# Performance work log

Hardware: AMD Instinct MI355X
Metric: run time of the kernel (lower is better)

Reference implementation:

```python
import jax, jax.numpy as jnp
import numpy as np

N_NODES = 50000


def _sage_mean(x, src, dst, Wl, bl, Wr, n_nodes):
    # PyG SAGEConv (aggr='mean', root_weight=True): lin_l(mean_j x_j) + lin_r(x_i)
    msgs = x[src]                                             # [E, F] gather
    agg = jax.ops.segment_sum(msgs, dst, num_segments=n_nodes)  # [N, F]
    cnt = jax.ops.segment_sum(jnp.ones((src.shape[0],), x.dtype), dst,
                              num_segments=n_nodes)           # [N]
    mean = agg / jnp.maximum(cnt, 1.0)[:, None]
    return mean @ Wl + bl + x @ Wr


def setup_inputs() -> dict:
    key = jax.random.key(0)
    ks = jax.random.split(key, 12)
    in_ft = 64
    o0, o1, o2 = 64, 128, 128
    d2 = o0 + o0          # conv2 in = 128
    d3 = o0 + o0 + o1     # conv3 in = 256
    E = 800000

    def lin(k, fi, fo):
        s = 1.0 / np.sqrt(fi)
        return jax.random.uniform(k, (fi, fo), jnp.float32, -s, s)

    x = jax.random.normal(ks[0], (N_NODES, in_ft), jnp.float32)
    edge_index = jax.random.randint(ks[1], (2, E), 0, N_NODES, jnp.int64)
    return {
        "x": x,
        "edge_index": edge_index,
        "Wp": lin(ks[2], in_ft, o0), "bp": jnp.zeros((o0,), jnp.float32),
        "Wl1": lin(ks[3], in_ft, o0), "bl1": jnp.zeros((o0,), jnp.float32),
        "Wr1": lin(ks[4], in_ft, o0),
        "Wl2": lin(ks[5], d2, o1), "bl2": jnp.zeros((o1,), jnp.float32),
        "Wr2": lin(ks[6], d2, o1),
        "Wl3": lin(ks[7], d3, o2), "bl3": jnp.zeros((o2,), jnp.float32),
        "Wr3": lin(ks[8], d3, o2),
    }


def reference(x, edge_index, Wp, bp, Wl1, bl1, Wr1, Wl2, bl2, Wr2, Wl3, bl3, Wr3):
    src, dst = edge_index[0], edge_index[1]
    act = jax.nn.relu
    x_p = act(x @ Wp + bp)                                        # [N, o0]
    h1 = act(_sage_mean(x, src, dst, Wl1, bl1, Wr1, N_NODES))      # [N, o0]
    in2 = jnp.concatenate([x_p, h1], axis=1)                      # [N, 2*o0]
    h2 = act(_sage_mean(in2, src, dst, Wl2, bl2, Wr2, N_NODES))    # [N, o1]
    in3 = jnp.concatenate([x_p, h1, h2], axis=1)                  # [N, 2*o0+o1]
    h3 = act(_sage_mean(in3, src, dst, Wl3, bl3, Wr3, N_NODES))    # [N, o2]
    return h3
```

## Files before the change

kernel.cpp:

```cpp
#include <hip/hip_runtime.h>

#define N_NODES 50000
#define ELLW 48
#define BINCAP 131072

typedef unsigned int uint;
typedef unsigned short ushort;
typedef float floatx4 __attribute__((ext_vector_type(4)));
typedef short short8 __attribute__((ext_vector_type(8)));

__device__ inline ushort f2bf(float f) {
    uint u = __float_as_uint(f);
    return (ushort)((u + 0x7fffu + ((u >> 16) & 1u)) >> 16);
}
__device__ inline float bflo(uint u) { return __uint_as_float(u << 16); }
__device__ inline float bfhi(uint u) { return __uint_as_float(u & 0xffff0000u); }

__device__ inline void swz_body(const float* __restrict__ W, ushort* __restrict__ Wz,
                                int O, int t) {
    int lane = t & 63, cb = t >> 6;
    int NBm = O / 16;
    int c = cb / NBm, nb = cb % NBm;
    int quad = lane >> 4, l16 = lane & 15;
#pragma unroll
    for (int j = 0; j < 8; j++) {
        float v = W[(size_t)(c * 32 + quad * 8 + j) * O + nb * 16 + l16];
        Wz[(size_t)t * 8 + j] = f2bf(v);
    }
}

__device__ void gemm1_body(int gb, const float* __restrict__ x,
                           const float* __restrict__ Wp, const float* __restrict__ bp,
                           ushort* __restrict__ feats, ushort* ldsA) {
    constexpr int LDA = 40;
    const int tid = threadIdx.x;
    const int wave = tid >> 6, lane = tid & 63;
    const int quad = lane >> 4, l16 = lane & 15;
    const int node0 = gb * 64;

    floatx4 acc[4];
#pragma unroll
    for (int nb = 0; nb < 4; nb++) acc[nb] = (floatx4){0, 0, 0, 0};

#pragma unroll
    for (int kk = 0; kk < 2; kk++) {
        const int k0 = kk * 32;
        __syncthreads();
        {
            int row = tid >> 2, seg = tid & 3;
            int node = node0 + row;
            float4 v0 = {0, 0, 0, 0}, v1 = {0, 0, 0, 0};
            if (node < N_NODES) {
                v0 = *(const float4*)&x[(size_t)node * 64 + k0 + seg * 8];
                v1 = *(const float4*)&x[(size_t)node * 64 + k0 + seg * 8 + 4];
            }
            ushort4 o0, o1;
            o0.x = f2bf(v0.x); o0.y = f2bf(v0.y); o0.z = f2bf(v0.z); o0.w = f2bf(v0.w);
            o1.x = f2bf(v1.x); o1.y = f2bf(v1.y); o1.z = f2bf(v1.z); o1.w = f2bf(v1.w);
            *(ushort4*)&ldsA[row * LDA + seg * 8] = o0;
            *(ushort4*)&ldsA[row * LDA + seg * 8 + 4] = o1;
        }
        __syncthreads();

        short8 a = *(const short8*)&ldsA[(wave * 16 + l16) * LDA + quad * 8];
#pragma unroll
        for (int nb = 0; nb < 4; nb++) {
            short8 bw;
#pragma unroll
            for (int j = 0; j < 8; j++)
                bw[j] = (short)f2bf(Wp[(size_t)(k0 + quad * 8 + j) * 64 + nb * 16 + l16]);
            acc[nb] = __builtin_amdgcn_mfma_f32_16x16x32_bf16(a, bw, acc[nb], 0, 0, 0);
        }
    }

#pragma unroll
    for (int nb = 0; nb < 4; nb++) {
        int ncol = nb * 16 + l16;
        float bv = bp[ncol];
#pragma unroll
        for (int r = 0; r < 4; r++) {
            int node = node0 + wave * 16 + quad * 4 + r;
            if (node >= N_NODES) continue;
            feats[(size_t)node * 256 + ncol] = f2bf(fmaxf(acc[nb][r] + bv, 0.f));
        }
    }
}

__global__ __launch_bounds__(256) void k1_mega(
    const int* __restrict__ src, const int* __restrict__ dst, int E,
    uint* __restrict__ bins, int* __restrict__ binCnt, int* __restrict__ fillc,
    const float* __restrict__ x, ushort* __restrict__ xb,
    const float* __restrict__ Wp, const float* __restrict__ bp, ushort* __restrict__ feats,
    const float* __restrict__ Wl1, ushort* __restrict__ zl1,
    const float* __restrict__ Wr1, ushort* __restrict__ zr1,
    const float* __restrict__ Wl2, ushort* __restrict__ zl2,
    const float* __restrict__ Wr2, ushort* __restrict__ zr2,
    const float* __restrict__ Wl3, ushort* __restrict__ zl3,
    const float* __restrict__ Wr3, ushort* __restrict__ zr3,
    int NA, int NG, int NC, int NZ)
{
    __shared__ ushort ldsA[64 * 40];
    __shared__ int cnt[8], base[8];
    int b = blockIdx.x, tid = threadIdx.x;

    if (b < NA) {
        int t = b * 256 + tid;
        bool valid = t < E;
        int s = 0, d = 0, bin = 0;
        if (valid) { s = src[t]; d = dst[t]; bin = d / 6250; }
        if (tid < 8) cnt[tid] = 0;
        __syncthreads();
        int rank = 0;
        if (valid) rank = atomicAdd(&cnt[bin], 1);
        __syncthreads();
        if (tid < 8) base[tid] = atomicAdd(&binCnt[tid], cnt[tid]);
        __syncthreads();
        if (valid)
            bins[(size_t)bin * BINCAP + base[bin] + rank] = (uint)s | ((uint)d << 16);
        return;
    }
    b -= NA;
    if (b < NG) { gemm1_body(b, x, Wp, bp, feats, ldsA); return; }
    b -= NG;
    if (b < NC) {
        int t = b * 256 + tid;
        float4 v = ((const float4*)x)[t];
        ushort4 o;
        o.x = f2bf(v.x); o.y = f2bf(v.y); o.z = f2bf(v.z); o.w = f2bf(v.w);
        ((ushort4*)xb)[t] = o;
        return;
    }
    b -= NC;
    if (b < NZ) {
        int t = b * 256 + tid;
        if (t < 12500) ((uint4*)fillc)[t] = (uint4){0, 0, 0, 0};
        return;
    }
    b -= NZ;
    if      (b < 2)  swz_body(Wl1, zl1, 64,  (b - 0) * 256 + tid);
    else if (b < 4)  swz_body(Wr1, zr1, 64,  (b - 2) * 256 + tid);
    else if (b < 12) swz_body(Wl2, zl2, 128, (b - 4) * 256 + tid);
    else if (b < 20) swz_body(Wr2, zr2, 128, (b - 12) * 256 + tid);
    else if (b < 36) swz_body(Wl3, zl3, 128, (b - 20) * 256 + tid);
    else             swz_body(Wr3, zr3, 128, (b - 36) * 256 + tid);
}

__global__ __launch_bounds__(256) void scatter_k(const uint* __restrict__ bins,
                                                 const int* __restrict__ binCnt,
                                                 int* __restrict__ fillc,
                                                 ushort* __restrict__ ell) {
    int bin = blockIdx.x & 7;
    int sub = blockIdx.x >> 3;
    int n = binCnt[bin];
    const uint* bp = bins + (size_t)bin * BINCAP;
    for (int i = sub * 256 + threadIdx.x; i < n; i += 64 * 256) {
        uint pk = bp[i];
        int s = pk & 0xFFFF, d = pk >> 16;
        int p = atomicAdd(&fillc[d], 1);
        if (p < ELLW) ell[(size_t)d * ELLW + p] = (ushort)s;
    }
}


__global__ __launch_bounds__(256) void gather64_k(const int* __restrict__ fillc,
                                                  const ushort* __restrict__ ell,
                                                  const ushort* __restrict__ in,
                                                  ushort* __restrict__ out) {
    int wid = blockIdx.x * 4 + (threadIdx.x >> 6);
    int lane = threadIdx.x & 63;
    int half = lane >> 5;
    int node = wid * 2 + half;
    if (node >= N_NODES) return;
    int l32 = lane & 31;
    int sub = l32 >> 3, c = l32 & 7;
    int n = fillc[node]; int nc = (n > ELLW) ? ELLW : n;
    const ushort* base = ell + (size_t)node * ELLW;
    float a[8];
#pragma unroll
    for (int j = 0; j < 8; j++) a[j] = 0.f;

    int i = sub;
    for (; i + 12 < nc; i += 16) {
        uint4 u0 = *(const uint4*)&in[(size_t)base[i] * 64 + 8 * c];
        uint4 u1 = *(const uint4*)&in[(size_t)base[i + 4] * 64 + 8 * c];
        uint4 u2 = *(const uint4*)&in[(size_t)base[i + 8] * 64 + 8 * c];
        uint4 u3 = *(const uint4*)&in[(size_t)base[i + 12] * 64 + 8 * c];
        a[0] += (bflo(u0.x) + bflo(u1.x)) + (bflo(u2.x) + bflo(u3.x));
        a[1] += (bfhi(u0.x) + bfhi(u1.x)) + (bfhi(u2.x) + bfhi(u3.x));
        a[2] += (bflo(u0.y) + bflo(u1.y)) + (bflo(u2.y) + bflo(u3.y));
        a[3] += (bfhi(u0.y) + bfhi(u1.y)) + (bfhi(u2.y) + bfhi(u3.y));
        a[4] += (bflo(u0.z) + bflo(u1.z)) + (bflo(u2.z) + bflo(u3.z));
        a[5] += (bfhi(u0.z) + bfhi(u1.z)) + (bfhi(u2.z) + bfhi(u3.z));
        a[6] += (bflo(u0.w) + bflo(u1.w)) + (bflo(u2.w) + bflo(u3.w));
        a[7] += (bfhi(u0.w) + bfhi(u1.w)) + (bfhi(u2.w) + bfhi(u3.w));
    }
    for (; i < nc; i += 4) {
        uint4 u0 = *(const uint4*)&in[(size_t)base[i] * 64 + 8 * c];
        a[0] += bflo(u0.x);  a[1] += bfhi(u0.x);
        a[2] += bflo(u0.y);  a[3] += bfhi(u0.y);
        a[4] += bflo(u0.z);  a[5] += bfhi(u0.z);
        a[6] += bflo(u0.w);  a[7] += bfhi(u0.w);
    }
#pragma unroll
    for (int j = 0; j < 8; j++) {
        a[j] += __shfl_xor(a[j], 8);
        a[j] += __shfl_xor(a[j], 16);
    }
    if (sub == 0) {
        float iv = 1.0f / fmaxf((float)n, 1.0f);
        uint4 r;
        r.x = (uint)f2bf(a[0] * iv) | ((uint)f2bf(a[1] * iv) << 16);
        r.y = (uint)f2bf(a[2] * iv) | ((uint)f2bf(a[3] * iv) << 16);
        r.z = (uint)f2bf(a[4] * iv) | ((uint)f2bf(a[5] * iv) << 16);
        r.w = (uint)f2bf(a[6] * iv) | ((uint)f2bf(a[7] * iv) << 16);
        *(uint4*)&out[(size_t)node * 64 + 8 * c] = r;
    }
}

__global__ __launch_bounds__(256) void gather128_k(const int* __restrict__ fillc,
                                                   const ushort* __restrict__ ell,
                                                   const ushort* __restrict__ in,
                                                   ushort* __restrict__ out) {
    int node = blockIdx.x * 4 + (threadIdx.x >> 6);
    if (node >= N_NODES) return;
    int lane = threadIdx.x & 63;
    int sub = lane >> 4, c = lane & 15;
    int n = fillc[node]; int nc = (n > ELLW) ? ELLW : n;
    const ushort* base = ell + (size_t)node * ELLW;
    float a[8];
#pragma unroll
    for (int j = 0; j < 8; j++) a[j] = 0.f;

    int i = sub;
    for (; i + 12 < nc; i += 16) {
        uint4 u0 = *(const uint4*)&in[(size_t)base[i] * 256 + 8 * c];
        uint4 u1 = *(const uint4*)&in[(size_t)base[i + 4] * 256 + 8 * c];
        uint4 u2 = *(const uint4*)&in[(size_t)base[i + 8] * 256 + 8 * c];
        uint4 u3 = *(const uint4*)&in[(size_t)base[i + 12] * 256 + 8 * c];
        a[0] += (bflo(u0.x) + bflo(u1.x)) + (bflo(u2.x) + bflo(u3.x));
        a[1] += (bfhi(u0.x) + bfhi(u1.x)) + (bfhi(u2.x) + bfhi(u3.x));
        a[2] += (bflo(u0.y) + bflo(u1.y)) + (bflo(u2.y) + bflo(u3.y));
        a[3] += (bfhi(u0.y) + bfhi(u1.y)) + (bfhi(u2.y) + bfhi(u3.y));
        a[4] += (bflo(u0.z) + bflo(u1.z)) + (bflo(u2.z) + bflo(u3.z));
        a[5] += (bfhi(u0.z) + bfhi(u1.z)) + (bfhi(u2.z) + bfhi(u3.z));
        a[6] += (bflo(u0.w) + bflo(u1.w)) + (bflo(u2.w) + bflo(u3.w));
        a[7] += (bfhi(u0.w) + bfhi(u1.w)) + (bfhi(u2.w) + bfhi(u3.w));
    }
    for (; i < nc; i += 4) {
        uint4 u0 = *(const uint4*)&in[(size_t)base[i] * 256 + 8 * c];
        a[0] += bflo(u0.x);  a[1] += bfhi(u0.x);
        a[2] += bflo(u0.y);  a[3] += bfhi(u0.y);
        a[4] += bflo(u0.z);  a[5] += bfhi(u0.z);
        a[6] += bflo(u0.w);  a[7] += bfhi(u0.w);
    }
#pragma unroll
    for (int j = 0; j < 8; j++) {
        a[j] += __shfl_xor(a[j], 16);
        a[j] += __shfl_xor(a[j], 32);
    }
    if (sub == 0) {
        float iv = 1.0f / fmaxf((float)n, 1.0f);
        uint4 r;
        r.x = (uint)f2bf(a[0] * iv) | ((uint)f2bf(a[1] * iv) << 16);
        r.y = (uint)f2bf(a[2] * iv) | ((uint)f2bf(a[3] * iv) << 16);
        r.z = (uint)f2bf(a[4] * iv) | ((uint)f2bf(a[5] * iv) << 16);
        r.w = (uint)f2bf(a[6] * iv) | ((uint)f2bf(a[7] * iv) << 16);
        *(uint4*)&out[(size_t)node * 256 + 8 * c] = r;
    }
}


template <int O, bool OUT_BF16>
__global__ __launch_bounds__(256) void mfma_gemm_k(
    const ushort* __restrict__ A1, int s1, int K1, const ushort* __restrict__ Wz1,
    const ushort* __restrict__ A2, int s2, int K2, const ushort* __restrict__ Wz2,
    const float* __restrict__ bias, void* __restrict__ outp, int so, int ocol)
{
    constexpr int NB = O / 16;
    constexpr int LDA = 40;
    __shared__ ushort ldsA[64 * LDA];

    const int tid = threadIdx.x;
    const int wave = tid >> 6, lane = tid & 63;
    const int quad = lane >> 4, l16 = lane & 15;
    const int node0 = blockIdx.x * 64;

    floatx4 acc[NB];
#pragma unroll
    for (int nb = 0; nb < NB; nb++) acc[nb] = (floatx4){0, 0, 0, 0};

#pragma unroll 1
    for (int phase = 0; phase < 2; ++phase) {
        const ushort* A = phase ? A2 : A1;
        const ushort* Wz = phase ? Wz2 : Wz1;
        const int K = phase ? K2 : K1;
        const int sA = phase ? s2 : s1;

#pragma unroll 1
        for (int k0 = 0; k0 < K; k0 += 32) {
            __syncthreads();
            {
                int row = tid >> 2, seg = tid & 3;
                int node = node0 + row;
                uint4 v = {0, 0, 0, 0};
                if (node < N_NODES)
                    v = *(const uint4*)&A[(size_t)node * sA + k0 + seg * 8];
                *(uint4*)&ldsA[row * LDA + seg * 8] = v;
            }
            __syncthreads();

            short8 a = *(const short8*)&ldsA[(wave * 16 + l16) * LDA + quad * 8];
            const short8* bz = (const short8*)Wz + (size_t)(k0 >> 5) * NB * 64;
#pragma unroll
            for (int nb = 0; nb < NB; nb++) {
                short8 b = bz[nb * 64 + lane];
                acc[nb] = __builtin_amdgcn_mfma_f32_16x16x32_bf16(a, b, acc[nb], 0, 0, 0);
            }
        }
    }

#pragma unroll
    for (int nb = 0; nb < NB; nb++) {
        int ncol = nb * 16 + l16;
        float bv = bias[ncol];
#pragma unroll
        for (int r = 0; r < 4; r++) {
            int node = node0 + wave * 16 + quad * 4 + r;
            if (node >= N_NODES) continue;
            float v = fmaxf(acc[nb][r] + bv, 0.f);
            if (OUT_BF16)
                ((ushort*)outp)[(size_t)node * so + ocol + ncol] = f2bf(v);
            else
                ((float*)outp)[(size_t)node * so + ocol + ncol] = v;
        }
    }
}


extern "C" void kernel_launch(void* const* d_in, const int* in_sizes, int n_in,
                              void* d_out, int out_size, void* d_ws, size_t ws_size,
                              hipStream_t stream) {
    const float* x   = (const float*)d_in[0];
    const int*   ei  = (const int*)d_in[1];
    const float* Wp  = (const float*)d_in[2];
    const float* bp  = (const float*)d_in[3];
    const float* Wl1 = (const float*)d_in[4];
    const float* bl1 = (const float*)d_in[5];
    const float* Wr1 = (const float*)d_in[6];
    const float* Wl2 = (const float*)d_in[7];
    const float* bl2 = (const float*)d_in[8];
    const float* Wr2 = (const float*)d_in[9];
    const float* Wl3 = (const float*)d_in[10];
    const float* bl3 = (const float*)d_in[11];
    const float* Wr3 = (const float*)d_in[12];

    const int E = in_sizes[1] / 2;
    const int N = N_NODES;
    const int* src = ei;
    const int* dst = ei + E;

    char* p = (char*)d_ws;
    ushort* xb    = (ushort*)p;  p += (size_t)N * 64 * 2;
    ushort* feats = (ushort*)p;  p += (size_t)N * 256 * 2;
    ushort* aggx  = (ushort*)p;  p += (size_t)N * 64 * 2;
    ushort* aggf  = (ushort*)p;  p += (size_t)N * 256 * 2;
    int* fillc    = (int*)p;     p += (size_t)N * 4;
    ushort* ell   = (ushort*)p;  p += (size_t)N * ELLW * 2;
    uint* bins    = (uint*)p;    p += (size_t)8 * BINCAP * 4;
    int* binCnt   = (int*)p;     p += 16 * 4;
    ushort* zl1   = (ushort*)p;  p += 64 * 64 * 2;
    ushort* zr1   = (ushort*)p;  p += 64 * 64 * 2;
    ushort* zl2   = (ushort*)p;  p += 128 * 128 * 2;
    ushort* zr2   = (ushort*)p;  p += 128 * 128 * 2;
    ushort* zl3   = (ushort*)p;  p += 256 * 128 * 2;
    ushort* zr3   = (ushort*)p;  p += 256 * 128 * 2;

    hipMemsetAsync(binCnt, 0, 16 * sizeof(int), stream);

    const int NA = (E + 255) / 256;
    const int NG = (N + 63) / 64;
    const int NC = (N * 64 / 4) / 256;
    const int NZ = 49;

    k1_mega<<<NA + NG + NC + NZ + 52, 256, 0, stream>>>(
        src, dst, E, bins, binCnt, fillc, x, xb, Wp, bp, feats,
        Wl1, zl1, Wr1, zr1, Wl2, zl2, Wr2, zr2, Wl3, zl3, Wr3, zr3,
        NA, NG, NC, NZ);

    scatter_k<<<512, 256, 0, stream>>>(bins, binCnt, fillc, ell);

    gather64_k<<<(N + 7) / 8, 256, 0, stream>>>(fillc, ell, xb, aggx);

    mfma_gemm_k<64, true><<<NG, 256, 0, stream>>>(
        aggx, 64, 64, zl1, xb, 64, 64, zr1, bl1, feats, 256, 64);

    gather128_k<<<(N + 3) / 4, 256, 0, stream>>>(fillc, ell, feats, aggf);

    mfma_gemm_k<128, true><<<NG, 256, 0, stream>>>(
        aggf, 256, 128, zl2, feats, 256, 128, zr2, bl2, feats, 256, 128);

    gather128_k<<<(N + 3) / 4, 256, 0, stream>>>(fillc, ell, feats + 128, aggf + 128);

    mfma_gemm_k<128, false><<<NG, 256, 0, stream>>>(
        aggf, 256, 256, zl3, feats, 256, 256, zr3, bl3, (float*)d_out, 128, 0);
}
```

Baseline: 306.7 us.

## Move per-node slot atomics into binning pass and fuse bf16 x conversion into GEMM1

The per-destination fill-counter atomic moves from the scatter kernel into the first (binning) pass, so each binned edge now carries its precomputed ELL slot, and scatter becomes plain stores. Fill counters are zeroed with one memset together with the bin counters. The separate x-to-bf16 conversion blocks are dropped because gemm1 already converts x and now also writes xb. Scatter is launched with more blocks. In exchange, bin entries double in size to 8 bytes, and the global atomics now run in the first pass, which is more scattered.

```diff
diff --git a/kernel.cpp b/kernel.cpp
--- a/kernel.cpp
+++ b/kernel.cpp
@@ -31,7 +31,8 @@
 
 __device__ void gemm1_body(int gb, const float* __restrict__ x,
                            const float* __restrict__ Wp, const float* __restrict__ bp,
-                           ushort* __restrict__ feats, ushort* ldsA) {
+                           ushort* __restrict__ feats, ushort* __restrict__ xb,
+                           ushort* ldsA) {
     constexpr int LDA = 40;
     const int tid = threadIdx.x;
     const int wave = tid >> 6, lane = tid & 63;
@@ -59,6 +60,10 @@
             o1.x = f2bf(v1.x); o1.y = f2bf(v1.y); o1.z = f2bf(v1.z); o1.w = f2bf(v1.w);
             *(ushort4*)&ldsA[row * LDA + seg * 8] = o0;
             *(ushort4*)&ldsA[row * LDA + seg * 8 + 4] = o1;
+            if (node < N_NODES) {
+                *(ushort4*)&xb[(size_t)node * 64 + k0 + seg * 8] = o0;
+                *(ushort4*)&xb[(size_t)node * 64 + k0 + seg * 8 + 4] = o1;
+            }
         }
         __syncthreads();
 
@@ -88,7 +93,7 @@
 
 __global__ __launch_bounds__(256) void k1_mega(
     const int* __restrict__ src, const int* __restrict__ dst, int E,
-    uint* __restrict__ bins, int* __restrict__ binCnt, int* __restrict__ fillc,
+    uint2* __restrict__ bins, int* __restrict__ binCnt, int* __restrict__ fillc,
     const float* __restrict__ x, ushort* __restrict__ xb,
     const float* __restrict__ Wp, const float* __restrict__ bp, ushort* __restrict__ feats,
     const float* __restrict__ Wl1, ushort* __restrict__ zl1,
@@ -97,7 +102,7 @@
     const float* __restrict__ Wr2, ushort* __restrict__ zr2,
     const float* __restrict__ Wl3, ushort* __restrict__ zl3,
     const float* __restrict__ Wr3, ushort* __restrict__ zr3,
-    int NA, int NG, int NC, int NZ)
+    int NA, int NG)
 {
     __shared__ ushort ldsA[64 * 40];
     __shared__ int cnt[8], base[8];
@@ -106,37 +111,29 @@
     if (b < NA) {
         int t = b * 256 + tid;
         bool valid = t < E;
-        int s = 0, d = 0, bin = 0;
+        int s = 0, d = 0, bin = 0, p = 0;
         if (valid) { s = src[t]; d = dst[t]; bin = d / 6250; }
         if (tid < 8) cnt[tid] = 0;
         __syncthreads();
         int rank = 0;
-        if (valid) rank = atomicAdd(&cnt[bin], 1);
+        if (valid) {
+            rank = atomicAdd(&cnt[bin], 1);
+            p = atomicAdd(&fillc[d], 1);
+        }
         __syncthreads();
         if (tid < 8) base[tid] = atomicAdd(&binCnt[tid], cnt[tid]);
         __syncthreads();
-        if (valid)
-            bins[(size_t)bin * BINCAP + base[bin] + rank] = (uint)s | ((uint)d << 16);
+        if (valid) {
+            uint2 pk;
+            pk.x = (uint)s | ((uint)p << 16);
+            pk.y = (uint)d;
+            bins[(size_t)bin * BINCAP + base[bin] + rank] = pk;
+        }
         return;
     }
     b -= NA;
-    if (b < NG) { gemm1_body(b, x, Wp, bp, feats, ldsA); return; }
+    if (b < NG) { gemm1_body(b, x, Wp, bp, feats, xb, ldsA); return; }
     b -= NG;
-    if (b < NC) {
-        int t = b * 256 + tid;
-        float4 v = ((const float4*)x)[t];
-        ushort4 o;
-        o.x = f2bf(v.x); o.y = f2bf(v.y); o.z = f2bf(v.z); o.w = f2bf(v.w);
-        ((ushort4*)xb)[t] = o;
-        return;
-    }
-    b -= NC;
-    if (b < NZ) {
-        int t = b * 256 + tid;
-        if (t < 12500) ((uint4*)fillc)[t] = (uint4){0, 0, 0, 0};
-        return;
-    }
-    b -= NZ;
     if      (b < 2)  swz_body(Wl1, zl1, 64,  (b - 0) * 256 + tid);
     else if (b < 4)  swz_body(Wr1, zr1, 64,  (b - 2) * 256 + tid);
     else if (b < 12) swz_body(Wl2, zl2, 128, (b - 4) * 256 + tid);
@@ -145,18 +142,16 @@
     else             swz_body(Wr3, zr3, 128, (b - 36) * 256 + tid);
 }
 
-__global__ __launch_bounds__(256) void scatter_k(const uint* __restrict__ bins,
+__global__ __launch_bounds__(256) void scatter_k(const uint2* __restrict__ bins,
                                                  const int* __restrict__ binCnt,
-                                                 int* __restrict__ fillc,
                                                  ushort* __restrict__ ell) {
     int bin = blockIdx.x & 7;
     int sub = blockIdx.x >> 3;
     int n = binCnt[bin];
-    const uint* bp = bins + (size_t)bin * BINCAP;
-    for (int i = sub * 256 + threadIdx.x; i < n; i += 64 * 256) {
-        uint pk = bp[i];
-        int s = pk & 0xFFFF, d = pk >> 16;
-        int p = atomicAdd(&fillc[d], 1);
+    const uint2* bp = bins + (size_t)bin * BINCAP;
+    for (int i = sub * 256 + threadIdx.x; i < n; i += 256 * 256) {
+        uint2 pk = bp[i];
+        int s = pk.x & 0xFFFF, p = pk.x >> 16, d = (int)pk.y;
         if (p < ELLW) ell[(size_t)d * ELLW + p] = (ushort)s;
     }
 }
@@ -365,9 +360,9 @@
     ushort* aggx  = (ushort*)p;  p += (size_t)N * 64 * 2;
     ushort* aggf  = (ushort*)p;  p += (size_t)N * 256 * 2;
     int* fillc    = (int*)p;     p += (size_t)N * 4;
+    int* binCnt   = (int*)p;     p += 16 * 4;
     ushort* ell   = (ushort*)p;  p += (size_t)N * ELLW * 2;
-    uint* bins    = (uint*)p;    p += (size_t)8 * BINCAP * 4;
-    int* binCnt   = (int*)p;     p += 16 * 4;
+    uint2* bins   = (uint2*)p;   p += (size_t)8 * BINCAP * 8;
     ushort* zl1   = (ushort*)p;  p += 64 * 64 * 2;
     ushort* zr1   = (ushort*)p;  p += 64 * 64 * 2;
     ushort* zl2   = (ushort*)p;  p += 128 * 128 * 2;
@@ -375,19 +370,17 @@
     ushort* zl3   = (ushort*)p;  p += 256 * 128 * 2;
     ushort* zr3   = (ushort*)p;  p += 256 * 128 * 2;
 
-    hipMemsetAsync(binCnt, 0, 16 * sizeof(int), stream);
+    hipMemsetAsync(fillc, 0, ((size_t)N + 16) * sizeof(int), stream);
 
     const int NA = (E + 255) / 256;
     const int NG = (N + 63) / 64;
-    const int NC = (N * 64 / 4) / 256;
-    const int NZ = 49;
-
-    k1_mega<<<NA + NG + NC + NZ + 52, 256, 0, stream>>>(
+
+    k1_mega<<<NA + NG + 52, 256, 0, stream>>>(
         src, dst, E, bins, binCnt, fillc, x, xb, Wp, bp, feats,
         Wl1, zl1, Wr1, zr1, Wl2, zl2, Wr2, zr2, Wl3, zl3, Wr3, zr3,
-        NA, NG, NC, NZ);
-
-    scatter_k<<<512, 256, 0, stream>>>(bins, binCnt, fillc, ell);
+        NA, NG);
+
+    scatter_k<<<2048, 256, 0, stream>>>(bins, binCnt, ell);
 
     gather64_k<<<(N + 7) / 8, 256, 0, stream>>>(fillc, ell, xb, aggx);
 
```

Result: faster. 293.8 us (-4.2%).
